# Kernel optimization log

Measured on AMD Instinct MI355X. Metric: run time of the kernel, lower is better.

Reference implementation:

```python
import jax, jax.numpy as jnp
import numpy as np

DIMS = [30, 64, 32, 16, 8, 2]

def _kaiming_uniform(key, fan_out, fan_in):
    # torch kaiming_uniform_ default: a=0 -> gain=sqrt(2), bound=gain*sqrt(3/fan_in)
    bound = np.sqrt(2.0) * np.sqrt(3.0 / fan_in)
    return jax.random.uniform(key, (fan_out, fan_in), jnp.float32, -bound, bound)

def setup_inputs() -> dict:
    key = jax.random.key(0)
    ks = jax.random.split(key, 6)
    inp = {"x": jax.random.normal(ks[0], (1000000, DIMS[0]), jnp.float32)}
    for i in range(5):
        inp[f"w{i+1}"] = _kaiming_uniform(ks[i + 1], DIMS[i + 1], DIMS[i])
        inp[f"b{i+1}"] = jnp.zeros((DIMS[i + 1],), jnp.float32)
    return inp

def reference(x, w1, b1, w2, b2, w3, b3, w4, b4, w5, b5):
    # quant/dequant stubs are identity in fp32 mode
    h = jax.nn.relu(x @ w1.T + b1)
    h = jax.nn.relu(h @ w2.T + b2)
    h = jax.nn.relu(h @ w3.T + b3)
    h = jax.nn.relu(h @ w4.T + b4)
    return h @ w5.T + b5
```

## Files before the change

kernel.cpp:

```cpp
#include <hip/hip_runtime.h>
#include <hip/hip_bf16.h>


typedef float        f32x4 __attribute__((ext_vector_type(4)));
typedef unsigned int u32x4 __attribute__((ext_vector_type(4)));
typedef short        s16x8 __attribute__((ext_vector_type(8)));

static __device__ __forceinline__ unsigned int pkbf(float a, float b) {
    unsigned int ua = __builtin_bit_cast(unsigned int, a) + 0x8000u;
    unsigned int ub = __builtin_bit_cast(unsigned int, b) + 0x8000u;
    return __builtin_amdgcn_perm(ub, ua, 0x07060302u);
}
static __device__ __forceinline__ unsigned int rp2(float a, float b) {
    return pkbf(fmaxf(a, 0.0f), fmaxf(b, 0.0f));
}
static __device__ __forceinline__ unsigned short f2bf(float f) {
    __hip_bfloat16 h = __float2bfloat16(f);
    unsigned short r;
    __builtin_memcpy(&r, &h, sizeof(r));
    return r;
}

#define MFMA(A, B, C) __builtin_amdgcn_mfma_f32_16x16x32_bf16((A), (B), (C), 0, 0, 0)

#define SLOT_B 4352

__global__ __launch_bounds__(256) void mlp_mfma_kernel(
    const float* __restrict__ x,
    const float* __restrict__ w1, const float* __restrict__ b1,
    const float* __restrict__ w2, const float* __restrict__ b2,
    const float* __restrict__ w3, const float* __restrict__ b3,
    const float* __restrict__ w4, const float* __restrict__ b4,
    const float* __restrict__ w5, const float* __restrict__ b5,
    float* __restrict__ out, int n)
{
    __shared__ __attribute__((aligned(16))) unsigned char ldsX[4][SLOT_B];

    const int lane = threadIdx.x & 63;
    const int wv   = threadIdx.x >> 6;
    const int g    = lane >> 4;
    const int ml   = lane & 15;

    unsigned char* myL = &ldsX[wv][0];

    *(unsigned int*)(myL + 4096 + lane * 4) = 0u;

    s16x8 A1[4], A2[2][2], A3, A4, A5;
    #pragma unroll
    for (int t = 0; t < 4; ++t) {
        #pragma unroll
        for (int i = 0; i < 8; ++i) {
            const int k = 4*g + (i & 3) + ((i >> 2) << 4);
            const int m = 16*t + ml;
            float v = (k < 30) ? w1[m*30 + k] : 0.0f;
            A1[t][i] = (short)f2bf(v);
        }
    }
    #pragma unroll
    for (int t = 0; t < 2; ++t)
        #pragma unroll
        for (int s = 0; s < 2; ++s)
            #pragma unroll
            for (int i = 0; i < 8; ++i) {
                const int k = 4*g + (i & 3) + ((i >> 2) << 4);
                A2[t][s][i] = (short)f2bf(w2[(16*t + ml)*64 + 32*s + k]);
            }
    #pragma unroll
    for (int i = 0; i < 8; ++i) {
        const int k = 4*g + (i & 3) + ((i >> 2) << 4);
        A3[i] = (short)f2bf(w3[ml*32 + k]);
        float v4 = 0.0f, v5 = 0.0f;
        if (ml < 8) v4 = (k < 16) ? w4[ml*16 + k] : ((k == 16) ? b4[ml] : 0.0f);
        if (ml < 2) v5 = (k <  8) ? w5[ml*8  + k] : ((k ==  8) ? b5[ml] : 0.0f);
        A4[i] = (short)f2bf(v4);
        A5[i] = (short)f2bf(v5);
    }
    f32x4 bias1[4], bias2[2], bias3;
    #pragma unroll
    for (int t = 0; t < 4; ++t)
        #pragma unroll
        for (int q = 0; q < 4; ++q)
            bias1[t][q] = b1[16*t + 4*g + q];
    #pragma unroll
    for (int t = 0; t < 2; ++t)
        #pragma unroll
        for (int q = 0; q < 4; ++q)
            bias2[t][q] = b2[16*t + 4*g + q];
    #pragma unroll
    for (int q = 0; q < 4; ++q)
        bias3[q] = b3[4*g + q];

    const int ntiles = (n + 15) >> 4;
    const int npairs = (ntiles + 1) >> 1;
    const int NW = gridDim.x * 4;
    const int p0 = blockIdx.x * 4 + wv;
    if (p0 >= npairs) return;

    const size_t xbytes = (size_t)n * 120;

    auto loadpair = [&](int pr, f32x4 r[4], int& delta) {
        size_t gb = (size_t)pr * 3840;
        if (gb + 4096 > xbytes) gb = xbytes - 4096;
        delta = (int)((size_t)pr * 3840 - gb);
        const unsigned char* gp = (const unsigned char*)x + gb + (size_t)lane * 16;
        r[0] = *(const f32x4*)(gp);
        r[1] = *(const f32x4*)(gp + 1024);
        r[2] = *(const f32x4*)(gp + 2048);
        r[3] = *(const f32x4*)(gp + 3072);
    };

    f32x4 rA[4], rB[4];
    int deltaA = 0, deltaB = 0;
    loadpair(p0, rA, deltaA);

    const f32x4 zero = {0.0f, 0.0f, 0.0f, 0.0f};

    for (int p = p0; p < npairs; p += NW) {
        {
            unsigned char* lp = myL + lane * 16;
            *(f32x4*)(lp)        = rA[0];
            *(f32x4*)(lp + 1024) = rA[1];
            *(f32x4*)(lp + 2048) = rA[2];
            *(f32x4*)(lp + 3072) = rA[3];
        }

        s16x8 B0[2];
        const bool fullpair = ((p + 1) * 32 <= n);
        if (fullpair) {
            const float* L = (const float*)(myL + deltaA);
            #pragma unroll
            for (int j = 0; j < 2; ++j) {
                const float* rp = L + (16*j + ml) * 30 + 4*g;
                float2 a01 = *(const float2*)(rp);
                float2 a23 = *(const float2*)(rp + 2);
                float2 b01 = *(const float2*)(rp + 16);
                float2 b23 = *(const float2*)(rp + 18);
                u32x4 u;
                u.x = pkbf(a01.x, a01.y); u.y = pkbf(a23.x, a23.y);
                u.z = pkbf(b01.x, b01.y); u.w = pkbf(b23.x, b23.y);
                B0[j] = __builtin_bit_cast(s16x8, u);
            }
        } else {
            #pragma unroll
            for (int j = 0; j < 2; ++j) {
                int row = p*32 + 16*j + ml;
                if (row >= n) row = n - 1;
                const float* rp = x + (size_t)row * 30 + 4*g;
                float2 a01 = *(const float2*)(rp);
                float2 a23 = *(const float2*)(rp + 2);
                float2 b01 = *(const float2*)(rp + 16);
                float2 b23 = (g < 3) ? *(const float2*)(rp + 18) : make_float2(0.f, 0.f);
                u32x4 u;
                u.x = pkbf(a01.x, a01.y); u.y = pkbf(a23.x, a23.y);
                u.z = pkbf(b01.x, b01.y); u.w = pkbf(b23.x, b23.y);
                B0[j] = __builtin_bit_cast(s16x8, u);
            }
        }

        const int pn = p + NW;
        if (pn < npairs) loadpair(pn, rB, deltaB);

        f32x4 c1[2][4];
        #pragma unroll
        for (int t = 0; t < 4; ++t)
            #pragma unroll
            for (int j = 0; j < 2; ++j)
                c1[j][t] = MFMA(A1[t], B0[j], bias1[t]);

        s16x8 B1[2][2];
        #pragma unroll
        for (int j = 0; j < 2; ++j)
            #pragma unroll
            for (int s = 0; s < 2; ++s) {
                u32x4 u;
                u.x = rp2(c1[j][2*s][0],     c1[j][2*s][1]);
                u.y = rp2(c1[j][2*s][2],     c1[j][2*s][3]);
                u.z = rp2(c1[j][2*s + 1][0], c1[j][2*s + 1][1]);
                u.w = rp2(c1[j][2*s + 1][2], c1[j][2*s + 1][3]);
                B1[j][s] = __builtin_bit_cast(s16x8, u);
            }
        f32x4 c2[2][2];
        #pragma unroll
        for (int t = 0; t < 2; ++t)
            #pragma unroll
            for (int j = 0; j < 2; ++j) {
                f32x4 a = bias2[t];
                #pragma unroll
                for (int s = 0; s < 2; ++s) a = MFMA(A2[t][s], B1[j][s], a);
                c2[j][t] = a;
            }

        f32x4 c3[2];
        #pragma unroll
        for (int j = 0; j < 2; ++j) {
            u32x4 u2;
            u2.x = rp2(c2[j][0][0], c2[j][0][1]);
            u2.y = rp2(c2[j][0][2], c2[j][0][3]);
            u2.z = rp2(c2[j][1][0], c2[j][1][1]);
            u2.w = rp2(c2[j][1][2], c2[j][1][3]);
            c3[j] = MFMA(A3, __builtin_bit_cast(s16x8, u2), bias3);
        }

        f32x4 c4[2];
        #pragma unroll
        for (int j = 0; j < 2; ++j) {
            u32x4 u3;
            u3.x = rp2(c3[j][0], c3[j][1]);
            u3.y = rp2(c3[j][2], c3[j][3]);
            u3.z = (g == 0) ? 0x3F80u : 0u;
            u3.w = 0u;
            c4[j] = MFMA(A4, __builtin_bit_cast(s16x8, u3), zero);
        }

        f32x4 c5[2];
        #pragma unroll
        for (int j = 0; j < 2; ++j) {
            u32x4 u4;
            u4.x = (g == 2) ? 0x3F80u : rp2(c4[j][0], c4[j][1]);
            u4.y = (g == 2) ? 0u      : rp2(c4[j][2], c4[j][3]);
            u4.z = 0u; u4.w = 0u;
            c5[j] = MFMA(A5, __builtin_bit_cast(s16x8, u4), zero);
        }

        #pragma unroll
        for (int j = 0; j < 2; ++j) {
            const int orow = (2*p + j)*16 + lane;
            if (lane < 16 && orow < n) {
                float2 o; o.x = c5[j][0]; o.y = c5[j][1];
                *(float2*)(out + (size_t)orow * 2) = o;
            }
        }

        #pragma unroll
        for (int q = 0; q < 4; ++q) rA[q] = rB[q];
        deltaA = deltaB;
    }
}

extern "C" void kernel_launch(void* const* d_in, const int* in_sizes, int n_in,
                              void* d_out, int out_size, void* d_ws, size_t ws_size,
                              hipStream_t stream) {
    const float* x  = (const float*)d_in[0];
    const float* w1 = (const float*)d_in[1];
    const float* b1 = (const float*)d_in[2];
    const float* w2 = (const float*)d_in[3];
    const float* b2 = (const float*)d_in[4];
    const float* w3 = (const float*)d_in[5];
    const float* b3 = (const float*)d_in[6];
    const float* w4 = (const float*)d_in[7];
    const float* b4 = (const float*)d_in[8];
    const float* w5 = (const float*)d_in[9];
    const float* b5 = (const float*)d_in[10];
    float* out = (float*)d_out;

    const int n = in_sizes[0] / 30;
    const int ntiles = (n + 15) >> 4;
    const int npairs = (ntiles + 1) >> 1;
    int blocks = (npairs + 3) / 4;
    if (blocks > 1280) blocks = 1280;

    mlp_mfma_kernel<<<blocks, 256, 0, stream>>>(
        x, w1, b1, w2, b2, w3, b3, w4, b4, w5, b5, out, n);
}
```

Measured before the change: 41.36 us.

## Double-buffer LDS staging and prefetch input two iterations ahead

Each wave's LDS staging slot becomes two ping-pong slots. The next pair's registers are written to the alternate slot while the current one is processed, and the global load for the pair two iterations ahead is issued right after. This deepens the prefetch pipeline and removes the rA/rB register copy, aiming to hide more global-load latency. It doubles LDS use per block and replaces one register buffer with another, which could affect occupancy.

```diff
diff --git a/kernel.cpp b/kernel.cpp
--- a/kernel.cpp
+++ b/kernel.cpp
@@ -34,7 +34,7 @@
     const float* __restrict__ w5, const float* __restrict__ b5,
     float* __restrict__ out, int n)
 {
-    __shared__ __attribute__((aligned(16))) unsigned char ldsX[4][SLOT_B];
+    __shared__ __attribute__((aligned(16))) unsigned char ldsX[4][2 * SLOT_B];
 
     const int lane = threadIdx.x & 63;
     const int wv   = threadIdx.x >> 6;
@@ -43,7 +43,8 @@
 
     unsigned char* myL = &ldsX[wv][0];
 
-    *(unsigned int*)(myL + 4096 + lane * 4) = 0u;
+    *(unsigned int*)(myL +          4096 + lane * 4) = 0u;
+    *(unsigned int*)(myL + SLOT_B + 4096 + lane * 4) = 0u;
 
     s16x8 A1[4], A2[2][2], A3, A4, A5;
     #pragma unroll
@@ -108,26 +109,28 @@
         r[2] = *(const f32x4*)(gp + 2048);
         r[3] = *(const f32x4*)(gp + 3072);
     };
-
-    f32x4 rA[4], rB[4];
+    auto writeslot = [&](const f32x4 r[4], int sl) {
+        unsigned char* lp = myL + sl * SLOT_B + lane * 16;
+        *(f32x4*)(lp)        = r[0];
+        *(f32x4*)(lp + 1024) = r[1];
+        *(f32x4*)(lp + 2048) = r[2];
+        *(f32x4*)(lp + 3072) = r[3];
+    };
+
+    f32x4 rT[4];
     int deltaA = 0, deltaB = 0;
-    loadpair(p0, rA, deltaA);
+    loadpair(p0, rT, deltaA);
+    writeslot(rT, 0);
+    if (p0 + NW < npairs) loadpair(p0 + NW, rT, deltaB);
 
     const f32x4 zero = {0.0f, 0.0f, 0.0f, 0.0f};
+    int s = 0;
 
     for (int p = p0; p < npairs; p += NW) {
-        {
-            unsigned char* lp = myL + lane * 16;
-            *(f32x4*)(lp)        = rA[0];
-            *(f32x4*)(lp + 1024) = rA[1];
-            *(f32x4*)(lp + 2048) = rA[2];
-            *(f32x4*)(lp + 3072) = rA[3];
-        }
-
         s16x8 B0[2];
         const bool fullpair = ((p + 1) * 32 <= n);
         if (fullpair) {
-            const float* L = (const float*)(myL + deltaA);
+            const float* L = (const float*)(myL + s * SLOT_B + deltaA);
             #pragma unroll
             for (int j = 0; j < 2; ++j) {
                 const float* rp = L + (16*j + ml) * 30 + 4*g;
@@ -157,8 +160,11 @@
             }
         }
 
-        const int pn = p + NW;
-        if (pn < npairs) loadpair(pn, rB, deltaB);
+        if (p + NW < npairs) {
+            writeslot(rT, s ^ 1);
+            deltaA = deltaB;
+            if (p + 2*NW < npairs) loadpair(p + 2*NW, rT, deltaB);
+        }
 
         f32x4 c1[2][4];
         #pragma unroll
@@ -171,13 +177,13 @@
         #pragma unroll
         for (int j = 0; j < 2; ++j)
             #pragma unroll
-            for (int s = 0; s < 2; ++s) {
+            for (int ss = 0; ss < 2; ++ss) {
                 u32x4 u;
-                u.x = rp2(c1[j][2*s][0],     c1[j][2*s][1]);
-                u.y = rp2(c1[j][2*s][2],     c1[j][2*s][3]);
-                u.z = rp2(c1[j][2*s + 1][0], c1[j][2*s + 1][1]);
-                u.w = rp2(c1[j][2*s + 1][2], c1[j][2*s + 1][3]);
-                B1[j][s] = __builtin_bit_cast(s16x8, u);
+                u.x = rp2(c1[j][2*ss][0],     c1[j][2*ss][1]);
+                u.y = rp2(c1[j][2*ss][2],     c1[j][2*ss][3]);
+                u.z = rp2(c1[j][2*ss + 1][0], c1[j][2*ss + 1][1]);
+                u.w = rp2(c1[j][2*ss + 1][2], c1[j][2*ss + 1][3]);
+                B1[j][ss] = __builtin_bit_cast(s16x8, u);
             }
         f32x4 c2[2][2];
         #pragma unroll
@@ -186,7 +192,7 @@
             for (int j = 0; j < 2; ++j) {
                 f32x4 a = bias2[t];
                 #pragma unroll
-                for (int s = 0; s < 2; ++s) a = MFMA(A2[t][s], B1[j][s], a);
+                for (int ss = 0; ss < 2; ++ss) a = MFMA(A2[t][ss], B1[j][ss], a);
                 c2[j][t] = a;
             }
 
@@ -231,9 +237,7 @@
             }
         }
 
-        #pragma unroll
-        for (int q = 0; q < 4; ++q) rA[q] = rB[q];
-        deltaA = deltaB;
+        s ^= 1;
     }
 }
 
```

Result: slower. 44.46 us (+7.5%).
